# Kernel tuning notes

Measured on AMD Instinct MI355X. Metric: run time of the kernel, lower is better.

## Reference

```python
import jax, jax.numpy as jnp
import numpy as np

N_NODES = 1_000_000
N_EDGES = 8_000_000
EMB = 64
CHANNELS = 2
C_DIM = EMB // CHANNELS
NEG_SLOPE = 0.01  # nn.LeakyReLU default
EPS = 1e-10


def setup_inputs() -> dict:
    key = jax.random.key(0)
    k1, k2, k3, k4, k5 = jax.random.split(key, 5)
    ego_emb = jax.random.normal(k1, (N_NODES, EMB), dtype=jnp.float32)
    W = jax.random.normal(k2, (CHANNELS, EMB, C_DIM), dtype=jnp.float32) * (1.0 / np.sqrt(EMB))
    b = jax.random.normal(k3, (CHANNELS, 1, C_DIM), dtype=jnp.float32) * 0.01
    row_indices = jax.random.randint(k4, (N_EDGES,), 0, N_NODES, dtype=jnp.int32)
    col_indices = jax.random.randint(k5, (N_EDGES,), 0, N_NODES, dtype=jnp.int32)
    return {"ego_emb": ego_emb, "W": W, "b": b,
            "row_indices": row_indices, "col_indices": col_indices}


def _channel_gat(ego_emb, Wc, bc, row, col, n_nodes):
    # project nodes to this disentangled channel: [N, c_dim]
    h = jax.nn.leaky_relu(ego_emb @ Wc + bc, NEG_SLOPE)
    h_row = h[row]                      # [E, c_dim] edge gather (dst)
    h_col = h[col]                      # [E, c_dim] edge gather (src)
    logits = jax.nn.leaky_relu(jnp.sum(h_row * h_col, axis=-1), NEG_SLOPE)  # [E]
    # edge softmax per destination row (numerically stable)
    row_max = jax.ops.segment_max(logits, row, num_segments=n_nodes)
    ex = jnp.exp(logits - row_max[row])
    denom = jax.ops.segment_sum(ex, row, num_segments=n_nodes)
    alpha = ex / (denom[row] + EPS)     # [E]
    # scatter-add weighted messages into destination rows
    return jax.ops.segment_sum(alpha[:, None] * h_col, row, num_segments=n_nodes)


def reference(ego_emb, W, b, row_indices, col_indices):
    outs = [
        _channel_gat(ego_emb, W[c], b[c], row_indices, col_indices, ego_emb.shape[0])
        for c in range(CHANNELS)
    ]
    return jnp.concatenate(outs, axis=-1)  # [N, emb_size]
```

## Files before the change

kernel.cpp:

```cpp
#include <hip/hip_runtime.h>
#include <hip/hip_fp16.h>
#include <stdint.h>

#define NEG_SLOPE 0.01f
#define EPSF 1e-10f
#define NB_SHIFT 11
#define NB_ROWS (1 << NB_SHIFT)
#define NB_MAX 512
#define BP_EPT 16
#define BP_EDGES (256 * BP_EPT)
#define CB_CAP 20480

__device__ __forceinline__ float lrelu(float x){
  return fmaxf(x, 0.f) + NEG_SLOPE * fminf(x, 0.f);
}

__device__ __forceinline__ unsigned pkh2(float a, float b){
  __half2 h = __floats2half2_rn(a, b);
  return __builtin_bit_cast(unsigned, h);
}

__device__ __forceinline__ float2 uph2(unsigned u){
  return __half22float2(__builtin_bit_cast(__half2, u));
}

__global__ void conv_wb(const float* __restrict__ W,
                        const float* __restrict__ b,
                        float* __restrict__ Wf, float* __restrict__ bf){
  int i = blockIdx.x * blockDim.x + threadIdx.x;
  for (int idx = i; idx < 64 * 64; idx += blockDim.x * gridDim.x){
    int k = idx >> 6, j = idx & 63;
    int c = j >> 5, jj = j & 31;
    Wf[idx] = W[c * 2048 + k * 32 + jj];
  }
  if (i < 64) bf[i] = b[i];
}

__global__ __launch_bounds__(256) void proj(const float* __restrict__ ego,
                                            const float* __restrict__ Wf,
                                            const float* __restrict__ bf,
                                            __half* __restrict__ h2, int N){
  int n = blockIdx.x * 256 + threadIdx.x;
  if (n >= N) return;
  float acc[64];
  #pragma unroll
  for (int j = 0; j < 64; j++) acc[j] = bf[j];
  const float4* ep = (const float4*)(ego + (size_t)n * 64);
  for (int kk = 0; kk < 16; kk++){
    float4 q = ep[kk];
    float ev[4] = {q.x, q.y, q.z, q.w};
    const float* wbase = Wf + kk * 4 * 64;
    #pragma unroll
    for (int t = 0; t < 4; t++){
      float ek = ev[t];
      const float* wrow = wbase + t * 64;
      #pragma unroll
      for (int j = 0; j < 64; j++) acc[j] = fmaf(ek, wrow[j], acc[j]);
    }
  }
  uint4* dst = (uint4*)(h2 + (size_t)n * 64);
  #pragma unroll
  for (int v = 0; v < 8; v++){
    uint4 o;
    o.x = pkh2(lrelu(acc[8 * v + 0]), lrelu(acc[8 * v + 1]));
    o.y = pkh2(lrelu(acc[8 * v + 2]), lrelu(acc[8 * v + 3]));
    o.z = pkh2(lrelu(acc[8 * v + 4]), lrelu(acc[8 * v + 5]));
    o.w = pkh2(lrelu(acc[8 * v + 6]), lrelu(acc[8 * v + 7]));
    dst[v] = o;
  }
}

__global__ __launch_bounds__(256) void bhist(const int* __restrict__ row,
                                             int* __restrict__ bcnt, int E, int nb){
  __shared__ int lh[NB_MAX];
  for (int i = threadIdx.x; i < nb; i += 256) lh[i] = 0;
  __syncthreads();
  int i = blockIdx.x * 256 + threadIdx.x;
  int stride = gridDim.x * 256;
  for (; i < E; i += stride) atomicAdd(&lh[row[i] >> NB_SHIFT], 1);
  __syncthreads();
  for (int j = threadIdx.x; j < nb; j += 256){
    int v = lh[j];
    if (v) atomicAdd(&bcnt[j], v);
  }
}

__global__ __launch_bounds__(512) void bscan(const int* __restrict__ bcnt,
                                             int* __restrict__ bbase,
                                             int* __restrict__ bcur, int nb){
  __shared__ int sh[NB_MAX];
  int t = threadIdx.x;
  int v = (t < nb) ? bcnt[t] : 0;
  sh[t] = v; __syncthreads();
  for (int off = 1; off < NB_MAX; off <<= 1){
    int a = (t >= off) ? sh[t - off] : 0;
    __syncthreads();
    sh[t] += a;
    __syncthreads();
  }
  if (t < nb){
    int e = sh[t] - v;
    bbase[t] = e;
    bcur[t] = e;
  }
}

__global__ __launch_bounds__(256) void binpairs(const int* __restrict__ row,
                                                const int* __restrict__ col,
                                                int* __restrict__ bcur,
                                                unsigned int* __restrict__ tmp,
                                                int E, int nb){
  __shared__ int lh[NB_MAX];
  __shared__ int lofs[NB_MAX];
  __shared__ int lbase[NB_MAX];
  __shared__ int wsum[256];
  __shared__ unsigned int sval[BP_EDGES];
  __shared__ unsigned int sdst[BP_EDGES];
  int t = threadIdx.x;
  for (int i = t; i < nb; i += 256) lh[i] = 0;
  __syncthreads();
  int e0 = blockIdx.x * BP_EDGES;
  int tot = E - e0; if (tot > BP_EDGES) tot = BP_EDGES;
  int r[BP_EPT], c[BP_EPT], mo[BP_EPT];
  #pragma unroll
  for (int k = 0; k < BP_EPT; k++){
    int e = e0 + k * 256 + t;
    if (e < E){
      r[k] = row[e];
      c[k] = col[e];
      mo[k] = atomicAdd(&lh[r[k] >> NB_SHIFT], 1);
    } else r[k] = -1;
  }
  __syncthreads();
  int c0 = (2 * t < nb) ? lh[2 * t] : 0;
  int c1 = (2 * t + 1 < nb) ? lh[2 * t + 1] : 0;
  int s = c0 + c1;
  wsum[t] = s; __syncthreads();
  for (int off = 1; off < 256; off <<= 1){
    int a = (t >= off) ? wsum[t - off] : 0;
    __syncthreads();
    wsum[t] += a;
    __syncthreads();
  }
  int tb = wsum[t] - s;
  if (2 * t < nb){
    lofs[2 * t] = tb;
    if (c0) lbase[2 * t] = atomicAdd(&bcur[2 * t], c0);
  }
  if (2 * t + 1 < nb){
    lofs[2 * t + 1] = tb + c0;
    if (c1) lbase[2 * t + 1] = atomicAdd(&bcur[2 * t + 1], c1);
  }
  __syncthreads();
  #pragma unroll
  for (int k = 0; k < BP_EPT; k++){
    if (r[k] >= 0){
      int b = r[k] >> NB_SHIFT;
      int slot = lofs[b] + mo[k];
      sval[slot] = ((unsigned int)(r[k] & (NB_ROWS - 1)) << 20) | (unsigned int)c[k];
      sdst[slot] = (unsigned int)(lbase[b] + mo[k]);
    }
  }
  __syncthreads();
  for (int i = t; i < tot; i += 256) tmp[sdst[i]] = sval[i];
}

__global__ __launch_bounds__(512) void csrbuild(const unsigned int* __restrict__ tmp,
                                                const int* __restrict__ bbase,
                                                const int* __restrict__ bcnt,
                                                int2* __restrict__ odeg,
                                                int* __restrict__ colp,
                                                int N){
  __shared__ int cnt[NB_ROWS];
  __shared__ int wsum[512];
  __shared__ int scol[CB_CAP];
  int b = blockIdx.x;
  int r0 = b << NB_SHIFT;
  int t = threadIdx.x;
  for (int i = t; i < NB_ROWS; i += 512) cnt[i] = 0;
  __syncthreads();
  int s = bbase[b];
  int cb = bcnt[b];
  int e = s + cb;
  for (int p = s + t; p < e; p += 512) atomicAdd(&cnt[tmp[p] >> 20], 1);
  __syncthreads();
  int base_i = t * 4;
  int dv[4], loc[4];
  int sum = 0;
  #pragma unroll
  for (int k = 0; k < 4; k++){
    dv[k] = cnt[base_i + k];
    loc[k] = sum;
    sum += dv[k];
  }
  wsum[t] = sum; __syncthreads();
  for (int off = 1; off < 512; off <<= 1){
    int a = (t >= off) ? wsum[t - off] : 0;
    __syncthreads();
    wsum[t] += a;
    __syncthreads();
  }
  int tbase = wsum[t] - sum;
  #pragma unroll
  for (int k = 0; k < 4; k++){
    int i = base_i + k;
    int o = tbase + loc[k];
    if (r0 + i < N) odeg[r0 + i] = make_int2(s + o, dv[k]);
    cnt[i] = o;
  }
  __syncthreads();
  if (cb <= CB_CAP){
    for (int p = s + t; p < e; p += 512){
      unsigned int v = tmp[p];
      int pos = atomicAdd(&cnt[v >> 20], 1);
      scol[pos] = (int)(v & 0xFFFFFu);
    }
    __syncthreads();
    for (int i = t; i < cb; i += 512) colp[s + i] = scol[i];
  } else {
    for (int p = s + t; p < e; p += 512){
      unsigned int v = tmp[p];
      int pos = atomicAdd(&cnt[v >> 20], 1);
      colp[s + pos] = (int)(v & 0xFFFFFu);
    }
  }
}

__global__ __launch_bounds__(256) void agg2(const __half* __restrict__ h2,
                                            const int2* __restrict__ odeg,
                                            const int* __restrict__ colp,
                                            float* __restrict__ out, int N){
  int n = blockIdx.x * 256 + threadIdx.x;
  if (n >= N) return;
  unsigned hrp[32];
  const uint4* hr4 = (const uint4*)(h2 + (size_t)n * 64);
  #pragma unroll
  for (int v = 0; v < 8; v++){
    uint4 q = hr4[v];
    hrp[4 * v + 0] = q.x; hrp[4 * v + 1] = q.y;
    hrp[4 * v + 2] = q.z; hrp[4 * v + 3] = q.w;
  }
  float acc[64];
  #pragma unroll
  for (int j = 0; j < 64; j++) acc[j] = 0.f;
  float l0 = 0.f, l1 = 0.f;
  int2 od = odeg[n];
  int s = od.x, d = od.y;
  for (int p = s; p < s + d; ++p){
    int c = colp[p];
    unsigned hcp[32];
    const uint4* hc4 = (const uint4*)(h2 + (size_t)c * 64);
    #pragma unroll
    for (int v = 0; v < 8; v++){
      uint4 q = hc4[v];
      hcp[4 * v + 0] = q.x; hcp[4 * v + 1] = q.y;
      hcp[4 * v + 2] = q.z; hcp[4 * v + 3] = q.w;
    }
    float dot0 = 0.f, dot1 = 0.f;
    #pragma unroll
    for (int i = 0; i < 16; i++){
      float2 a = uph2(hrp[i]);
      float2 b = uph2(hcp[i]);
      dot0 = fmaf(a.x, b.x, dot0);
      dot0 = fmaf(a.y, b.y, dot0);
    }
    #pragma unroll
    for (int i = 16; i < 32; i++){
      float2 a = uph2(hrp[i]);
      float2 b = uph2(hcp[i]);
      dot1 = fmaf(a.x, b.x, dot1);
      dot1 = fmaf(a.y, b.y, dot1);
    }
    float w0 = __expf(fminf(lrelu(dot0), 80.f));
    float w1 = __expf(fminf(lrelu(dot1), 80.f));
    l0 += w0; l1 += w1;
    #pragma unroll
    for (int i = 0; i < 16; i++){
      float2 b = uph2(hcp[i]);
      acc[2 * i + 0] = fmaf(w0, b.x, acc[2 * i + 0]);
      acc[2 * i + 1] = fmaf(w0, b.y, acc[2 * i + 1]);
    }
    #pragma unroll
    for (int i = 16; i < 32; i++){
      float2 b = uph2(hcp[i]);
      acc[2 * i + 0] = fmaf(w1, b.x, acc[2 * i + 0]);
      acc[2 * i + 1] = fmaf(w1, b.y, acc[2 * i + 1]);
    }
  }
  float inv0 = 1.f / (l0 + EPSF);
  float inv1 = 1.f / (l1 + EPSF);
  float4* op = (float4*)(out + (size_t)n * 64);
  #pragma unroll
  for (int v = 0; v < 16; v++){
    float sc = (v < 8) ? inv0 : inv1;
    float4 o;
    o.x = acc[4 * v + 0] * sc;
    o.y = acc[4 * v + 1] * sc;
    o.z = acc[4 * v + 2] * sc;
    o.w = acc[4 * v + 3] * sc;
    op[v] = o;
  }
}

extern "C" void kernel_launch(void* const* d_in, const int* in_sizes, int n_in,
                              void* d_out, int out_size, void* d_ws, size_t ws_size,
                              hipStream_t stream){
  const float* ego = (const float*)d_in[0];
  const float* W   = (const float*)d_in[1];
  const float* b   = (const float*)d_in[2];
  const int* row = (const int*)d_in[3];
  const int* col = (const int*)d_in[4];
  int N = in_sizes[0] / 64;
  int E = in_sizes[3];
  float* out = (float*)d_out;

  char* ws = (char*)d_ws;
  float* Wf = (float*)ws;
  float* bf = Wf + 4096;
  size_t off = 32768;
  __half* h2 = (__half*)(ws + off); off += (size_t)N * 64 * 2;
  int2* odeg = (int2*)(ws + off); off += (size_t)N * 8;
  int* bcnt  = (int*)(ws + off); off += NB_MAX * 4;
  int* bbase = (int*)(ws + off); off += NB_MAX * 4;
  int* bcur  = (int*)(ws + off); off += NB_MAX * 4;
  unsigned int* tmp = (unsigned int*)(ws + off); off += (size_t)E * 4;
  int* colp = (int*)(ws + off);

  int nb = (N + NB_ROWS - 1) >> NB_SHIFT;

  hipMemsetAsync(bcnt, 0, NB_MAX * 4, stream);
  conv_wb<<<16, 256, 0, stream>>>(W, b, Wf, bf);
  proj<<<(N + 255) / 256, 256, 0, stream>>>(ego, Wf, bf, h2, N);
  bhist<<<1024, 256, 0, stream>>>(row, bcnt, E, nb);
  bscan<<<1, NB_MAX, 0, stream>>>(bcnt, bbase, bcur, nb);
  binpairs<<<(E + BP_EDGES - 1) / BP_EDGES, 256, 0, stream>>>(row, col, bcur, tmp, E, nb);
  csrbuild<<<nb, 512, 0, stream>>>(tmp, bbase, bcnt, odeg, colp, N);
  agg2<<<(N + 255) / 256, 256, 0, stream>>>(h2, odeg, colp, out, N);
}
```

Measured before the change: 1.026 ms.

## Degree-sort nodes within chunks to balance aggregation warp work

New measurement: 1.080 ms. +5.3%, slower.

```diff
diff --git a/kernel.cpp b/kernel.cpp
--- a/kernel.cpp
+++ b/kernel.cpp
@@ -9,7 +9,8 @@
 #define NB_MAX 512
 #define BP_EPT 16
 #define BP_EDGES (256 * BP_EPT)
-#define CB_CAP 20480
+#define CB_CAP 17408
+#define DS_NODES 4096
 
 __device__ __forceinline__ float lrelu(float x){
   return fmaxf(x, 0.f) + NEG_SLOPE * fminf(x, 0.f);
@@ -42,13 +43,16 @@
                                             __half* __restrict__ h2, int N){
   int n = blockIdx.x * 256 + threadIdx.x;
   if (n >= N) return;
+  const float4* ep = (const float4*)(ego + (size_t)n * 64);
+  float4 rowv[16];
+  #pragma unroll
+  for (int kk = 0; kk < 16; kk++) rowv[kk] = ep[kk];
   float acc[64];
   #pragma unroll
   for (int j = 0; j < 64; j++) acc[j] = bf[j];
-  const float4* ep = (const float4*)(ego + (size_t)n * 64);
+  #pragma unroll
   for (int kk = 0; kk < 16; kk++){
-    float4 q = ep[kk];
-    float ev[4] = {q.x, q.y, q.z, q.w};
+    float ev[4] = {rowv[kk].x, rowv[kk].y, rowv[kk].z, rowv[kk].w};
     const float* wbase = Wf + kk * 4 * 64;
     #pragma unroll
     for (int t = 0; t < 4; t++){
@@ -226,12 +230,57 @@
   }
 }
 
+__global__ __launch_bounds__(256) void dsort(const int2* __restrict__ odeg,
+                                             int* __restrict__ perm, int N){
+  __shared__ int hist[256];
+  __shared__ int wsum[256];
+  __shared__ int sperm[DS_NODES];
+  int t = threadIdx.x;
+  int base = blockIdx.x * DS_NODES;
+  int cnt = N - base; if (cnt > DS_NODES) cnt = DS_NODES;
+  hist[t] = 0;
+  __syncthreads();
+  int rk[16], bn[16];
+  #pragma unroll
+  for (int k = 0; k < 16; k++){
+    int i = k * 256 + t;
+    if (i < cnt){
+      int d = odeg[base + i].y;
+      bn[k] = d > 255 ? 255 : d;
+      rk[k] = atomicAdd(&hist[bn[k]], 1);
+    } else bn[k] = -1;
+  }
+  __syncthreads();
+  int h = hist[t];
+  wsum[t] = h; __syncthreads();
+  for (int off = 1; off < 256; off <<= 1){
+    int a = (t >= off) ? wsum[t - off] : 0;
+    __syncthreads();
+    wsum[t] += a;
+    __syncthreads();
+  }
+  __syncthreads();
+  hist[t] = wsum[t] - h;
+  __syncthreads();
+  #pragma unroll
+  for (int k = 0; k < 16; k++){
+    if (bn[k] >= 0){
+      int i = k * 256 + t;
+      sperm[hist[bn[k]] + rk[k]] = base + i;
+    }
+  }
+  __syncthreads();
+  for (int i = t; i < cnt; i += 256) perm[base + i] = sperm[i];
+}
+
 __global__ __launch_bounds__(256) void agg2(const __half* __restrict__ h2,
                                             const int2* __restrict__ odeg,
                                             const int* __restrict__ colp,
+                                            const int* __restrict__ perm,
                                             float* __restrict__ out, int N){
-  int n = blockIdx.x * 256 + threadIdx.x;
-  if (n >= N) return;
+  int i0 = blockIdx.x * 256 + threadIdx.x;
+  if (i0 >= N) return;
+  int n = perm[i0];
   unsigned hrp[32];
   const uint4* hr4 = (const uint4*)(h2 + (size_t)n * 64);
   #pragma unroll
@@ -320,6 +369,7 @@
   size_t off = 32768;
   __half* h2 = (__half*)(ws + off); off += (size_t)N * 64 * 2;
   int2* odeg = (int2*)(ws + off); off += (size_t)N * 8;
+  int* perm  = (int*)(ws + off); off += (size_t)N * 4;
   int* bcnt  = (int*)(ws + off); off += NB_MAX * 4;
   int* bbase = (int*)(ws + off); off += NB_MAX * 4;
   int* bcur  = (int*)(ws + off); off += NB_MAX * 4;
@@ -335,5 +385,6 @@
   bscan<<<1, NB_MAX, 0, stream>>>(bcnt, bbase, bcur, nb);
   binpairs<<<(E + BP_EDGES - 1) / BP_EDGES, 256, 0, stream>>>(row, col, bcur, tmp, E, nb);
   csrbuild<<<nb, 512, 0, stream>>>(tmp, bbase, bcnt, odeg, colp, N);
-  agg2<<<(N + 255) / 256, 256, 0, stream>>>(h2, odeg, colp, out, N);
-}
+  dsort<<<(N + DS_NODES - 1) / DS_NODES, 256, 0, stream>>>(odeg, perm, N);
+  agg2<<<(N + 255) / 256, 256, 0, stream>>>(h2, odeg, colp, perm, out, N);
+}
```
